# Performance work log

Measured on AMD Instinct MI355X. Metric: run time of the kernel, lower is better.

The kernel has to match this reference:

```python
import jax, jax.numpy as jnp
import numpy as np

H = 8      # num_attention_heads
DH = 96    # attention_head_size
LN_EPS = 1e-5


def setup_inputs() -> dict:
    key = jax.random.key(0)
    ks = jax.random.split(key, 12)
    B, S, D = 2, 768, 768
    sc = 0.02
    return {
        "hidden_states": jax.random.normal(ks[0], (B, S, D), jnp.float32),
        "distance_matrix": jax.random.uniform(ks[1], (B, S, S), jnp.float32) * 20.0,
        "angle_matrix": jax.random.uniform(ks[2], (B, S, S), jnp.float32) * np.pi,
        "attention_mask": jnp.ones((B, S), jnp.float32),
        "Wq": jax.random.normal(ks[3], (D, D), jnp.float32) * sc,
        "bq": jnp.zeros((D,), jnp.float32),
        "Wk": jax.random.normal(ks[4], (D, D), jnp.float32) * sc,
        "bk": jnp.zeros((D,), jnp.float32),
        "Wv": jax.random.normal(ks[5], (D, D), jnp.float32) * sc,
        "bv": jnp.zeros((D,), jnp.float32),
        "Wd": jax.random.normal(ks[6], (DH,), jnp.float32) * sc,
        "bd": jnp.zeros((DH,), jnp.float32),
        "Wa": jax.random.normal(ks[7], (DH,), jnp.float32) * sc,
        "ba": jnp.zeros((DH,), jnp.float32),
        "Wo": jax.random.normal(ks[8], (D, D), jnp.float32) * sc,
        "bo": jnp.zeros((D,), jnp.float32),
        "ln_g": jnp.ones((D,), jnp.float32),
        "ln_b": jnp.zeros((D,), jnp.float32),
    }


def _heads(x, B, S):
    # [B,S,D] -> [B,H,S,DH]
    return x.reshape(B, S, H, DH).transpose(0, 2, 1, 3)


def reference(hidden_states, distance_matrix, angle_matrix, attention_mask,
              Wq, bq, Wk, bk, Wv, bv, Wd, bd, Wa, ba, Wo, bo, ln_g, ln_b):
    B, S, D = hidden_states.shape
    q = _heads(hidden_states @ Wq.T + bq, B, S)   # [B,H,S,DH]
    k = _heads(hidden_states @ Wk.T + bk, B, S)
    v = _heads(hidden_states @ Wv.T + bv, B, S)

    scores = jnp.einsum('bhid,bhjd->bhij', q, k) / jnp.sqrt(jnp.float32(DH))

    # distance / angle relative-position biases: emb[b,i,j,:] = dist[b,i,j]*Wd + bd
    dist_emb = distance_matrix[..., None] * Wd + bd   # [B,S,S,DH]
    scores = scores + jnp.einsum('bhid,bijd->bhij', q, dist_emb)
    ang_emb = angle_matrix[..., None] * Wa + ba       # [B,S,S,DH]
    scores = scores + jnp.einsum('bhid,bijd->bhij', q, ang_emb)

    # key mask, broadcast over heads and query positions
    scores = scores + (1.0 - attention_mask)[:, None, None, :] * -10000.0

    probs = jax.nn.softmax(scores, axis=-1)           # [B,H,S,S]
    ctx = jnp.einsum('bhij,bhjd->bhid', probs, v)
    ctx = ctx.transpose(0, 2, 1, 3).reshape(B, S, D)  # [B,S,D]

    out = ctx @ Wo.T + bo
    x = out + hidden_states
    mu = jnp.mean(x, axis=-1, keepdims=True)
    var = jnp.var(x, axis=-1, keepdims=True)
    out = (x - mu) * jax.lax.rsqrt(var + LN_EPS) * ln_g + ln_b
    return out, probs
```

## Files before the change

kernel.cpp:

```cpp
#include <hip/hip_runtime.h>
#include <stdint.h>

#define B_  2
#define S_  768
#define D_  768
#define H_  8
#define DH_ 96

typedef unsigned short ushort_t;
typedef __bf16 bf16x8 __attribute__((ext_vector_type(8)));
typedef float  f32x4  __attribute__((ext_vector_type(4)));

__device__ inline ushort_t f2bf(float f) {
    union { float f; unsigned int u; } v; v.f = f;
    unsigned int u = v.u;
    unsigned int r = u + 0x7fffu + ((u >> 16) & 1u);
    return (ushort_t)(r >> 16);
}
__device__ inline float bf2f(ushort_t u) {
    union { unsigned int i; float f; } c; c.i = ((unsigned int)u) << 16;
    return c.f;
}

__device__ inline void glds16(const void* gp, void* lp) {
    auto g = reinterpret_cast<const __attribute__((address_space(1))) uint32_t*>(
        reinterpret_cast<uintptr_t>(gp));
    auto l = reinterpret_cast<__attribute__((address_space(3))) uint32_t*>(
        reinterpret_cast<uintptr_t>(lp));
    __builtin_amdgcn_global_load_lds(g, l, 16, 0, 0);
}

__global__ __launch_bounds__(256) void k_convert(
        const float* __restrict__ X, const float* __restrict__ Wq,
        const float* __restrict__ Wk, const float* __restrict__ Wv,
        const float* __restrict__ Wo,
        ushort_t* __restrict__ Xb, ushort_t* __restrict__ Wb) {
    const int NX4 = (B_ * S_ * D_) / 4;
    const int NW4 = (D_ * D_) / 4;
    int i = blockIdx.x * blockDim.x + threadIdx.x;
    float4 v;
    ushort_t* dst;
    if (i < NX4) {
        v = ((const float4*)X)[i];
        dst = Xb + i * 4;
    } else {
        int wi = i - NX4;
        int sel = wi / NW4;
        int off = wi - sel * NW4;
        const float* src = (sel == 0) ? Wq : (sel == 1) ? Wk : (sel == 2) ? Wv : Wo;
        v = ((const float4*)src)[off];
        dst = Wb + wi * 4;
    }
    ushort4 o;
    o.x = f2bf(v.x); o.y = f2bf(v.y); o.z = f2bf(v.z); o.w = f2bf(v.w);
    *(ushort4*)dst = o;
}

__device__ inline void gemm64_glds(
        const ushort_t* __restrict__ A, int lda,
        const ushort_t* __restrict__ Bt, int ldb,
        int K, int m0, int n0,
        ushort_t* As, ushort_t* Bs, f32x4 acc[2][2]) {
    const int tid  = threadIdx.x;
    const int lane = tid & 63, wave = tid >> 6;
    const int wm = (wave >> 1) * 32, wn = (wave & 1) * 32;
    const int fr = lane & 15, fk = (lane >> 4) * 8;
    const int sr = wave * 16 + (lane >> 2);
    const int sc = (lane & 3) * 8;
    const ushort_t* Ap = A  + (size_t)(m0 + sr) * lda + sc;
    const ushort_t* Bp = Bt + (size_t)(n0 + sr) * ldb + sc;
    ushort_t* AsW = As + wave * 512;
    ushort_t* BsW = Bs + wave * 512;
    for (int kt = 0; kt < K; kt += 32) {
        if (kt) __syncthreads();
        glds16(Ap + kt, AsW);
        glds16(Bp + kt, BsW);
        __syncthreads();
        bf16x8 a0 = *(const bf16x8*)&As[(wm      + fr) * 32 + fk];
        bf16x8 a1 = *(const bf16x8*)&As[(wm + 16 + fr) * 32 + fk];
        bf16x8 b0 = *(const bf16x8*)&Bs[(wn      + fr) * 32 + fk];
        bf16x8 b1 = *(const bf16x8*)&Bs[(wn + 16 + fr) * 32 + fk];
        acc[0][0] = __builtin_amdgcn_mfma_f32_16x16x32_bf16(a0, b0, acc[0][0], 0, 0, 0);
        acc[0][1] = __builtin_amdgcn_mfma_f32_16x16x32_bf16(a0, b1, acc[0][1], 0, 0, 0);
        acc[1][0] = __builtin_amdgcn_mfma_f32_16x16x32_bf16(a1, b0, acc[1][0], 0, 0, 0);
        acc[1][1] = __builtin_amdgcn_mfma_f32_16x16x32_bf16(a1, b1, acc[1][1], 0, 0, 0);
    }
}

__global__ __launch_bounds__(256) void k_qkv(
        const ushort_t* __restrict__ Xb, const ushort_t* __restrict__ Wb,
        const float* __restrict__ bq, const float* __restrict__ bk,
        const float* __restrict__ bv,
        ushort_t* __restrict__ Qb, ushort_t* __restrict__ Kb,
        ushort_t* __restrict__ Vtb) {
    __shared__ __align__(16) ushort_t As[128 * 32];
    __shared__ __align__(16) ushort_t Bs[64 * 32];
    f32x4 acc[4][2];
    #pragma unroll
    for (int i = 0; i < 4; i++)
        #pragma unroll
        for (int j = 0; j < 2; j++) acc[i][j] = (f32x4){0.f, 0.f, 0.f, 0.f};
    const int tid = threadIdx.x, lane = tid & 63, wave = tid >> 6;
    const int m0 = blockIdx.y * 128, n0 = blockIdx.x * 64;
    const int fr = lane & 15, fk = (lane >> 4) * 8;
    const int wm = (wave >> 1) * 64, wn = (wave & 1) * 32;
    const int sr = lane >> 2, sc = (lane & 3) * 8;
    const ushort_t* Ap0 = Xb + (size_t)(m0 + wave * 32 + sr) * D_ + sc;
    const ushort_t* Ap1 = Ap0 + 16 * D_;
    const ushort_t* Bp  = Wb + (size_t)(n0 + wave * 16 + sr) * D_ + sc;
    ushort_t* AsW0 = As + wave * 1024;
    ushort_t* AsW1 = As + wave * 1024 + 512;
    ushort_t* BsW  = Bs + wave * 512;
    for (int kt = 0; kt < D_; kt += 32) {
        if (kt) __syncthreads();
        glds16(Ap0 + kt, AsW0);
        glds16(Ap1 + kt, AsW1);
        glds16(Bp  + kt, BsW);
        __syncthreads();
        bf16x8 a[4], b[2];
        #pragma unroll
        for (int mi = 0; mi < 4; mi++)
            a[mi] = *(const bf16x8*)&As[(wm + mi * 16 + fr) * 32 + fk];
        #pragma unroll
        for (int ni = 0; ni < 2; ni++)
            b[ni] = *(const bf16x8*)&Bs[(wn + ni * 16 + fr) * 32 + fk];
        #pragma unroll
        for (int mi = 0; mi < 4; mi++)
            #pragma unroll
            for (int ni = 0; ni < 2; ni++)
                acc[mi][ni] = __builtin_amdgcn_mfma_f32_16x16x32_bf16(a[mi], b[ni], acc[mi][ni], 0, 0, 0);
    }
    #pragma unroll
    for (int ni = 0; ni < 2; ni++) {
        int gcol = n0 + wn + ni * 16 + fr;
        int g = gcol / D_, d768 = gcol - g * D_;
        int h = d768 / DH_, d = d768 - h * DH_;
        float bias = (g == 0 ? bq : (g == 1 ? bk : bv))[d768];
        #pragma unroll
        for (int mi = 0; mi < 4; mi++) {
            #pragma unroll
            for (int r = 0; r < 4; r++) {
                int grow = m0 + wm + mi * 16 + (lane >> 4) * 4 + r;
                int bidx = grow / S_, s = grow - bidx * S_;
                ushort_t ob = f2bf(acc[mi][ni][r] + bias);
                int bh = bidx * H_ + h;
                if (g == 0)      Qb[((size_t)bh * S_ + s) * DH_ + d] = ob;
                else if (g == 1) Kb[((size_t)bh * S_ + s) * DH_ + d] = ob;
                else             Vtb[((size_t)bh * DH_ + d) * S_ + s] = ob;
            }
        }
    }
}

__global__ __launch_bounds__(256) void k_qcoef(
        const ushort_t* __restrict__ Qb,
        const float* __restrict__ Wd, const float* __restrict__ bd,
        const float* __restrict__ Wa, const float* __restrict__ ba,
        float* __restrict__ qcoef) {
    const int wave = threadIdx.x >> 6, lane = threadIdx.x & 63;
    const int row = blockIdx.x * 4 + wave;
    const ushort_t* q = Qb + (size_t)row * DH_;
    float e0 = bf2f(q[lane]);
    float c0 = e0 * Wd[lane];
    float c1 = e0 * Wa[lane];
    float c2 = e0 * (bd[lane] + ba[lane]);
    if (lane < 32) {
        int d = 64 + lane;
        float e1 = bf2f(q[d]);
        c0 += e1 * Wd[d];
        c1 += e1 * Wa[d];
        c2 += e1 * (bd[d] + ba[d]);
    }
    #pragma unroll
    for (int o = 32; o > 0; o >>= 1) {
        c0 += __shfl_down(c0, o);
        c1 += __shfl_down(c1, o);
        c2 += __shfl_down(c2, o);
    }
    if (lane == 0) {
        qcoef[row * 3 + 0] = c0;
        qcoef[row * 3 + 1] = c1;
        qcoef[row * 3 + 2] = c2;
    }
}

__global__ __launch_bounds__(256) void k_scores(
        const ushort_t* __restrict__ Qb, const ushort_t* __restrict__ Kb,
        const float* __restrict__ qcoef,
        const float* __restrict__ distm, const float* __restrict__ angm,
        const float* __restrict__ mask, float* __restrict__ Sc) {
    __shared__ __align__(16) ushort_t As[64 * 32];
    __shared__ __align__(16) ushort_t Bs[64 * 32];
    f32x4 acc[2][2];
    #pragma unroll
    for (int i = 0; i < 2; i++)
        #pragma unroll
        for (int j = 0; j < 2; j++) acc[i][j] = (f32x4){0.f, 0.f, 0.f, 0.f};
    const int bh = blockIdx.z, b = bh >> 3;
    const ushort_t* A  = Qb + (size_t)bh * S_ * DH_;
    const ushort_t* Bt = Kb + (size_t)bh * S_ * DH_;
    const int m0 = blockIdx.y * 64, n0 = blockIdx.x * 64;
    gemm64_glds(A, DH_, Bt, DH_, DH_, m0, n0, As, Bs, acc);
    const int lane = threadIdx.x & 63, wave = threadIdx.x >> 6;
    const int wm = (wave >> 1) * 32, wn = (wave & 1) * 32;
    const float isq = 0.10206207261596577f;
    #pragma unroll
    for (int ni = 0; ni < 2; ni++) {
        int j = n0 + wn + ni * 16 + (lane & 15);
        float mb = (1.0f - mask[b * S_ + j]) * -10000.0f;
        #pragma unroll
        for (int mi = 0; mi < 2; mi++) {
            #pragma unroll
            for (int r = 0; r < 4; r++) {
                int i = m0 + wm + mi * 16 + (lane >> 4) * 4 + r;
                const float* qc = qcoef + ((size_t)bh * S_ + i) * 3;
                float dist = distm[((size_t)b * S_ + i) * S_ + j];
                float ang  = angm [((size_t)b * S_ + i) * S_ + j];
                Sc[((size_t)bh * S_ + i) * S_ + j] =
                    acc[mi][ni][r] * isq + dist * qc[0] + ang * qc[1] + qc[2] + mb;
            }
        }
    }
}

__global__ __launch_bounds__(256) void k_attnctx(
        const float* __restrict__ Sc, const ushort_t* __restrict__ Vtb,
        float* __restrict__ probs, ushort_t* __restrict__ Ctxb) {
    const int bh = blockIdx.y, b = bh >> 3, h = bh & 7;
    const int r0 = blockIdx.x * 32;
    const float* S = Sc + ((size_t)bh * S_ + r0) * S_;
    const ushort_t* Vt = Vtb + (size_t)bh * DH_ * S_;
    __shared__ float mrow[32], lrow[32];
    __shared__ __align__(16) ushort_t Ps[32 * 32];
    __shared__ __align__(16) ushort_t Vs[96 * 32];
    const int tid = threadIdx.x, lane = tid & 63, wave = tid >> 6;
    for (int rr = 0; rr < 8; rr++) {
        int row = wave * 8 + rr;
        const float* sr = S + (size_t)row * S_;
        float4 x0 = ((const float4*)sr)[lane];
        float4 x1 = ((const float4*)sr)[lane + 64];
        float4 x2 = ((const float4*)sr)[lane + 128];
        float mx = fmaxf(fmaxf(fmaxf(x0.x, x0.y), fmaxf(x0.z, x0.w)),
                   fmaxf(fmaxf(fmaxf(x1.x, x1.y), fmaxf(x1.z, x1.w)),
                         fmaxf(fmaxf(x2.x, x2.y), fmaxf(x2.z, x2.w))));
        #pragma unroll
        for (int o = 32; o > 0; o >>= 1) mx = fmaxf(mx, __shfl_down(mx, o));
        mx = __shfl(mx, 0);
        float s = __expf(x0.x - mx) + __expf(x0.y - mx) + __expf(x0.z - mx) + __expf(x0.w - mx)
                + __expf(x1.x - mx) + __expf(x1.y - mx) + __expf(x1.z - mx) + __expf(x1.w - mx)
                + __expf(x2.x - mx) + __expf(x2.y - mx) + __expf(x2.z - mx) + __expf(x2.w - mx);
        #pragma unroll
        for (int o = 32; o > 0; o >>= 1) s += __shfl_down(s, o);
        if (lane == 0) { mrow[row] = mx; lrow[row] = s; }
    }
    __syncthreads();
    const int mrow0 = (wave & 1) * 16;
    const int nb    = (wave >> 1) * 48;
    const int fr = lane & 15, fk = (lane >> 4) * 8;
    const int prow = tid >> 3, pc = (tid & 7) * 4;
    const float pm = mrow[prow];
    const float pinvl = 1.0f / lrow[prow];
    f32x4 acc[3];
    #pragma unroll
    for (int i = 0; i < 3; i++) acc[i] = (f32x4){0.f, 0.f, 0.f, 0.f};
    const int vr0 = tid >> 2, vc0 = (tid & 3) * 8;
    const int i1 = tid + 256;
    const int vr1 = i1 >> 2, vc1 = (i1 & 3) * 8;
    for (int kt = 0; kt < S_; kt += 32) {
        if (kt) __syncthreads();
        {
            float4 s4 = *(const float4*)(S + (size_t)prow * S_ + kt + pc);
            float e0 = __expf(s4.x - pm), e1 = __expf(s4.y - pm);
            float e2 = __expf(s4.z - pm), e3 = __expf(s4.w - pm);
            ushort4 pb;
            pb.x = f2bf(e0); pb.y = f2bf(e1); pb.z = f2bf(e2); pb.w = f2bf(e3);
            *(ushort4*)&Ps[prow * 32 + pc] = pb;
            float4 pn = {e0 * pinvl, e1 * pinvl, e2 * pinvl, e3 * pinvl};
            *(float4*)&probs[((size_t)bh * S_ + r0 + prow) * S_ + kt + pc] = pn;
        }
        *(uint4*)&Vs[vr0 * 32 + vc0] = *(const uint4*)(Vt + (size_t)vr0 * S_ + kt + vc0);
        if (i1 < 384)
            *(uint4*)&Vs[vr1 * 32 + vc1] = *(const uint4*)(Vt + (size_t)vr1 * S_ + kt + vc1);
        __syncthreads();
        bf16x8 a = *(const bf16x8*)&Ps[(mrow0 + fr) * 32 + fk];
        #pragma unroll
        for (int ni = 0; ni < 3; ni++) {
            bf16x8 bfr = *(const bf16x8*)&Vs[(nb + ni * 16 + fr) * 32 + fk];
            acc[ni] = __builtin_amdgcn_mfma_f32_16x16x32_bf16(a, bfr, acc[ni], 0, 0, 0);
        }
    }
    #pragma unroll
    for (int ni = 0; ni < 3; ni++) {
        int col = nb + ni * 16 + fr;
        #pragma unroll
        for (int r = 0; r < 4; r++) {
            int row = mrow0 + (lane >> 4) * 4 + r;
            float o = acc[ni][r] / lrow[row];
            Ctxb[((size_t)(b * S_ + r0 + row)) * D_ + h * DH_ + col] = f2bf(o);
        }
    }
}

__global__ __launch_bounds__(256) void k_out(
        const ushort_t* __restrict__ Ctxb, const ushort_t* __restrict__ Wob,
        const float* __restrict__ bo, const float* __restrict__ hidden,
        float* __restrict__ xbuf) {
    __shared__ __align__(16) ushort_t As[64 * 32];
    __shared__ __align__(16) ushort_t Bs[64 * 32];
    f32x4 acc[2][2];
    #pragma unroll
    for (int i = 0; i < 2; i++)
        #pragma unroll
        for (int j = 0; j < 2; j++) acc[i][j] = (f32x4){0.f, 0.f, 0.f, 0.f};
    const int m0 = blockIdx.y * 64, n0 = blockIdx.x * 64;
    gemm64_glds(Ctxb, D_, Wob, D_, D_, m0, n0, As, Bs, acc);
    const int lane = threadIdx.x & 63, wave = threadIdx.x >> 6;
    const int wm = (wave >> 1) * 32, wn = (wave & 1) * 32;
    #pragma unroll
    for (int ni = 0; ni < 2; ni++) {
        int gcol = n0 + wn + ni * 16 + (lane & 15);
        float bias = bo[gcol];
        #pragma unroll
        for (int mi = 0; mi < 2; mi++) {
            #pragma unroll
            for (int r = 0; r < 4; r++) {
                int grow = m0 + wm + mi * 16 + (lane >> 4) * 4 + r;
                xbuf[(size_t)grow * D_ + gcol] =
                    acc[mi][ni][r] + bias + hidden[(size_t)grow * D_ + gcol];
            }
        }
    }
}

__global__ __launch_bounds__(256) void k_ln(
        const float* __restrict__ xbuf, const float* __restrict__ g,
        const float* __restrict__ bb, float* __restrict__ out) {
    const float* x = xbuf + (size_t)blockIdx.x * D_;
    const int t = threadIdx.x;
    float a0 = x[t], a1 = x[t + 256], a2 = x[t + 512];
    float s = a0 + a1 + a2;
    float ss = a0 * a0 + a1 * a1 + a2 * a2;
    __shared__ float r1[4], r2[4];
    #pragma unroll
    for (int o = 32; o > 0; o >>= 1) { s += __shfl_down(s, o); ss += __shfl_down(ss, o); }
    if ((t & 63) == 0) { r1[t >> 6] = s; r2[t >> 6] = ss; }
    __syncthreads();
    float ts = r1[0] + r1[1] + r1[2] + r1[3];
    float tss = r2[0] + r2[1] + r2[2] + r2[3];
    float mu = ts * (1.0f / D_);
    float var = tss * (1.0f / D_) - mu * mu;
    float rstd = rsqrtf(var + 1e-5f);
    float* o = out + (size_t)blockIdx.x * D_;
    o[t]       = (a0 - mu) * rstd * g[t]       + bb[t];
    o[t + 256] = (a1 - mu) * rstd * g[t + 256] + bb[t + 256];
    o[t + 512] = (a2 - mu) * rstd * g[t + 512] + bb[t + 512];
}

extern "C" void kernel_launch(void* const* d_in, const int* in_sizes, int n_in,
                              void* d_out, int out_size, void* d_ws, size_t ws_size,
                              hipStream_t stream) {
    const float* X     = (const float*)d_in[0];
    const float* distm = (const float*)d_in[1];
    const float* angm  = (const float*)d_in[2];
    const float* mask  = (const float*)d_in[3];
    const float* Wq    = (const float*)d_in[4];
    const float* bq    = (const float*)d_in[5];
    const float* Wk    = (const float*)d_in[6];
    const float* bk    = (const float*)d_in[7];
    const float* Wv    = (const float*)d_in[8];
    const float* bv    = (const float*)d_in[9];
    const float* Wd    = (const float*)d_in[10];
    const float* bd    = (const float*)d_in[11];
    const float* Wa    = (const float*)d_in[12];
    const float* ba    = (const float*)d_in[13];
    const float* Wo    = (const float*)d_in[14];
    const float* bo    = (const float*)d_in[15];
    const float* ln_g  = (const float*)d_in[16];
    const float* ln_b  = (const float*)d_in[17];

    float* outp  = (float*)d_out;
    float* probs = (float*)d_out + (size_t)B_ * S_ * D_;

    char* ws = (char*)d_ws;
    ushort_t* Xb    = (ushort_t*)(ws + 0);
    ushort_t* Wb    = (ushort_t*)(ws + 2359296);
    ushort_t* Qb    = (ushort_t*)(ws + 7077888);
    ushort_t* Kb    = (ushort_t*)(ws + 9437184);
    ushort_t* Vtb   = (ushort_t*)(ws + 11796480);
    ushort_t* Ctxb  = (ushort_t*)(ws + 14155776);
    float*    qcoef = (float*)   (ws + 16515072);
    float*    xbuf  = (float*)   (ws + 16662528);
    float*    Sc    = (float*)   (ws + 21381120);

    k_convert<<<3456, 256, 0, stream>>>(X, Wq, Wk, Wv, Wo, Xb, Wb);
    k_qkv<<<dim3(36, 12), 256, 0, stream>>>(Xb, Wb, bq, bk, bv, Qb, Kb, Vtb);
    k_qcoef<<<3072, 256, 0, stream>>>(Qb, Wd, bd, Wa, ba, qcoef);
    k_scores<<<dim3(12, 12, 16), 256, 0, stream>>>(Qb, Kb, qcoef, distm, angm, mask, Sc);
    k_attnctx<<<dim3(24, 16), 256, 0, stream>>>(Sc, Vtb, probs, Ctxb);
    k_out<<<dim3(12, 24), 256, 0, stream>>>(Ctxb, Wb + (size_t)2304 * 768, bo, X, xbuf);
    k_ln<<<1536, 256, 0, stream>>>(xbuf, ln_g, ln_b, outp);
}
```

Measured before the change: 206.7 us.

## Fuse score computation, softmax and PV into one register-resident attention kernel

Result: faster. 180.8 us (-12.5%).

```diff
diff --git a/kernel.cpp b/kernel.cpp
--- a/kernel.cpp
+++ b/kernel.cpp
@@ -93,57 +93,31 @@
         const float* __restrict__ bv,
         ushort_t* __restrict__ Qb, ushort_t* __restrict__ Kb,
         ushort_t* __restrict__ Vtb) {
-    __shared__ __align__(16) ushort_t As[128 * 32];
+    __shared__ __align__(16) ushort_t As[64 * 32];
     __shared__ __align__(16) ushort_t Bs[64 * 32];
-    f32x4 acc[4][2];
-    #pragma unroll
-    for (int i = 0; i < 4; i++)
+    f32x4 acc[2][2];
+    #pragma unroll
+    for (int i = 0; i < 2; i++)
         #pragma unroll
         for (int j = 0; j < 2; j++) acc[i][j] = (f32x4){0.f, 0.f, 0.f, 0.f};
-    const int tid = threadIdx.x, lane = tid & 63, wave = tid >> 6;
-    const int m0 = blockIdx.y * 128, n0 = blockIdx.x * 64;
-    const int fr = lane & 15, fk = (lane >> 4) * 8;
-    const int wm = (wave >> 1) * 64, wn = (wave & 1) * 32;
-    const int sr = lane >> 2, sc = (lane & 3) * 8;
-    const ushort_t* Ap0 = Xb + (size_t)(m0 + wave * 32 + sr) * D_ + sc;
-    const ushort_t* Ap1 = Ap0 + 16 * D_;
-    const ushort_t* Bp  = Wb + (size_t)(n0 + wave * 16 + sr) * D_ + sc;
-    ushort_t* AsW0 = As + wave * 1024;
-    ushort_t* AsW1 = As + wave * 1024 + 512;
-    ushort_t* BsW  = Bs + wave * 512;
-    for (int kt = 0; kt < D_; kt += 32) {
-        if (kt) __syncthreads();
-        glds16(Ap0 + kt, AsW0);
-        glds16(Ap1 + kt, AsW1);
-        glds16(Bp  + kt, BsW);
-        __syncthreads();
-        bf16x8 a[4], b[2];
-        #pragma unroll
-        for (int mi = 0; mi < 4; mi++)
-            a[mi] = *(const bf16x8*)&As[(wm + mi * 16 + fr) * 32 + fk];
-        #pragma unroll
-        for (int ni = 0; ni < 2; ni++)
-            b[ni] = *(const bf16x8*)&Bs[(wn + ni * 16 + fr) * 32 + fk];
-        #pragma unroll
-        for (int mi = 0; mi < 4; mi++)
-            #pragma unroll
-            for (int ni = 0; ni < 2; ni++)
-                acc[mi][ni] = __builtin_amdgcn_mfma_f32_16x16x32_bf16(a[mi], b[ni], acc[mi][ni], 0, 0, 0);
-    }
+    const int m0 = blockIdx.y * 64, n0 = blockIdx.x * 64;
+    gemm64_glds(Xb, D_, Wb, D_, D_, m0, n0, As, Bs, acc);
+    const int lane = threadIdx.x & 63, wave = threadIdx.x >> 6;
+    const int wm = (wave >> 1) * 32, wn = (wave & 1) * 32;
     #pragma unroll
     for (int ni = 0; ni < 2; ni++) {
-        int gcol = n0 + wn + ni * 16 + fr;
+        int gcol = n0 + wn + ni * 16 + (lane & 15);
         int g = gcol / D_, d768 = gcol - g * D_;
         int h = d768 / DH_, d = d768 - h * DH_;
         float bias = (g == 0 ? bq : (g == 1 ? bk : bv))[d768];
         #pragma unroll
-        for (int mi = 0; mi < 4; mi++) {
+        for (int mi = 0; mi < 2; mi++) {
             #pragma unroll
             for (int r = 0; r < 4; r++) {
                 int grow = m0 + wm + mi * 16 + (lane >> 4) * 4 + r;
-                int bidx = grow / S_, s = grow - bidx * S_;
+                int b = grow / S_, s = grow - b * S_;
                 ushort_t ob = f2bf(acc[mi][ni][r] + bias);
-                int bh = bidx * H_ + h;
+                int bh = b * H_ + h;
                 if (g == 0)      Qb[((size_t)bh * S_ + s) * DH_ + d] = ob;
                 else if (g == 1) Kb[((size_t)bh * S_ + s) * DH_ + d] = ob;
                 else             Vtb[((size_t)bh * DH_ + d) * S_ + s] = ob;
@@ -184,119 +158,174 @@
     }
 }
 
-__global__ __launch_bounds__(256) void k_scores(
+#define L1B 29696
+__global__ __launch_bounds__(256) void k_flash(
         const ushort_t* __restrict__ Qb, const ushort_t* __restrict__ Kb,
-        const float* __restrict__ qcoef,
+        const ushort_t* __restrict__ Vtb, const float* __restrict__ qcoef,
         const float* __restrict__ distm, const float* __restrict__ angm,
-        const float* __restrict__ mask, float* __restrict__ Sc) {
-    __shared__ __align__(16) ushort_t As[64 * 32];
-    __shared__ __align__(16) ushort_t Bs[64 * 32];
-    f32x4 acc[2][2];
-    #pragma unroll
-    for (int i = 0; i < 2; i++)
-        #pragma unroll
-        for (int j = 0; j < 2; j++) acc[i][j] = (f32x4){0.f, 0.f, 0.f, 0.f};
-    const int bh = blockIdx.z, b = bh >> 3;
-    const ushort_t* A  = Qb + (size_t)bh * S_ * DH_;
-    const ushort_t* Bt = Kb + (size_t)bh * S_ * DH_;
-    const int m0 = blockIdx.y * 64, n0 = blockIdx.x * 64;
-    gemm64_glds(A, DH_, Bt, DH_, DH_, m0, n0, As, Bs, acc);
-    const int lane = threadIdx.x & 63, wave = threadIdx.x >> 6;
-    const int wm = (wave >> 1) * 32, wn = (wave & 1) * 32;
+        const float* __restrict__ mask,
+        float* __restrict__ probs, ushort_t* __restrict__ Ctxb) {
+    __shared__ __align__(16) char sm[2 * L1B + 640];
+    float* mstat = (float*)(sm + 2 * L1B);
+    float* lstat = (float*)(sm + 2 * L1B + 256);
+    float* linv  = (float*)(sm + 2 * L1B + 512);
+    const int idx = blockIdx.x;
+    const int h = idx / 48, rem = idx - h * 48;
+    const int b = rem / 24, r0 = (rem - b * 24) * 32;
+    const int bh = b * H_ + h;
+    const int tid = threadIdx.x, lane = tid & 63, w = tid >> 6;
+    const int frn = lane & 15, fko = (lane >> 4) * 8, frg4 = (lane >> 4) * 4;
+    const int rg = w & 1, cp = w >> 1;
+    const ushort_t* Qbh = Qb + (size_t)bh * S_ * DH_;
+    const ushort_t* Kbh = Kb + (size_t)bh * S_ * DH_;
+    const ushort_t* Vbh = Vtb + (size_t)bh * DH_ * S_;
+
+    bf16x8 aq[3];
+    {
+        const ushort_t* qp = Qbh + (size_t)(r0 + rg * 16 + frn) * DH_ + fko;
+        aq[0] = *(const bf16x8*)qp;
+        aq[1] = *(const bf16x8*)(qp + 32);
+        aq[2] = *(const bf16x8*)(qp + 64);
+    }
+    float qc0[4], qc1[4], qc2[4];
+    #pragma unroll
+    for (int r = 0; r < 4; r++) {
+        const float* qp = qcoef + ((size_t)bh * S_ + r0 + rg * 16 + frg4 + r) * 3;
+        qc0[r] = qp[0]; qc1[r] = qp[1]; qc2[r] = qp[2];
+    }
     const float isq = 0.10206207261596577f;
-    #pragma unroll
-    for (int ni = 0; ni < 2; ni++) {
-        int j = n0 + wn + ni * 16 + (lane & 15);
-        float mb = (1.0f - mask[b * S_ + j]) * -10000.0f;
-        #pragma unroll
-        for (int mi = 0; mi < 2; mi++) {
+
+    f32x4 acc[24];
+    #pragma unroll
+    for (int c = 0; c < 12; ++c) {
+        char* bufc = sm + (c & 1) * L1B;
+        ushort_t* Ks = (ushort_t*)bufc;
+        float* Dd = (float*)(bufc + 12288);
+        float* Da = (float*)(bufc + 20992);
+        #pragma unroll
+        for (int k = 0; k < 3; ++k) {
+            int i = tid + 256 * k;
+            int row = i / 12, cc = (i - row * 12) * 8;
+            *(uint4*)(Ks + row * 96 + cc) =
+                *(const uint4*)(Kbh + (size_t)(c * 64 + row) * DH_ + cc);
+        }
+        #pragma unroll
+        for (int k = 0; k < 2; ++k) {
+            int i = tid + 256 * k;
+            int row = i >> 4, c4 = (i & 15) * 4;
+            size_t src = ((size_t)b * S_ + r0 + row) * S_ + c * 64 + c4;
+            *(float4*)(Dd + row * 68 + c4) = *(const float4*)(distm + src);
+            *(float4*)(Da + row * 68 + c4) = *(const float4*)(angm + src);
+        }
+        __syncthreads();
+        #pragma unroll
+        for (int tt = 0; tt < 2; ++tt) {
+            const ushort_t* kp = Ks + (cp * 32 + tt * 16 + frn) * 96 + fko;
+            f32x4 ca = (f32x4){0.f, 0.f, 0.f, 0.f};
+            ca = __builtin_amdgcn_mfma_f32_16x16x32_bf16(aq[0], *(const bf16x8*)kp, ca, 0, 0, 0);
+            ca = __builtin_amdgcn_mfma_f32_16x16x32_bf16(aq[1], *(const bf16x8*)(kp + 32), ca, 0, 0, 0);
+            ca = __builtin_amdgcn_mfma_f32_16x16x32_bf16(aq[2], *(const bf16x8*)(kp + 64), ca, 0, 0, 0);
+            int jl = cp * 32 + tt * 16 + frn;
+            float mb = (1.0f - mask[b * S_ + c * 64 + jl]) * -10000.0f;
             #pragma unroll
-            for (int r = 0; r < 4; r++) {
-                int i = m0 + wm + mi * 16 + (lane >> 4) * 4 + r;
-                const float* qc = qcoef + ((size_t)bh * S_ + i) * 3;
-                float dist = distm[((size_t)b * S_ + i) * S_ + j];
-                float ang  = angm [((size_t)b * S_ + i) * S_ + j];
-                Sc[((size_t)bh * S_ + i) * S_ + j] =
-                    acc[mi][ni][r] * isq + dist * qc[0] + ang * qc[1] + qc[2] + mb;
+            for (int r = 0; r < 4; ++r) {
+                int rl = rg * 16 + frg4 + r;
+                acc[c * 2 + tt][r] = ca[r] * isq + Dd[rl * 68 + jl] * qc0[r]
+                                   + Da[rl * 68 + jl] * qc1[r] + qc2[r] + mb;
             }
         }
     }
-}
-
-__global__ __launch_bounds__(256) void k_attnctx(
-        const float* __restrict__ Sc, const ushort_t* __restrict__ Vtb,
-        float* __restrict__ probs, ushort_t* __restrict__ Ctxb) {
-    const int bh = blockIdx.y, b = bh >> 3, h = bh & 7;
-    const int r0 = blockIdx.x * 32;
-    const float* S = Sc + ((size_t)bh * S_ + r0) * S_;
-    const ushort_t* Vt = Vtb + (size_t)bh * DH_ * S_;
-    __shared__ float mrow[32], lrow[32];
-    __shared__ __align__(16) ushort_t Ps[32 * 32];
-    __shared__ __align__(16) ushort_t Vs[96 * 32];
-    const int tid = threadIdx.x, lane = tid & 63, wave = tid >> 6;
-    for (int rr = 0; rr < 8; rr++) {
-        int row = wave * 8 + rr;
-        const float* sr = S + (size_t)row * S_;
-        float4 x0 = ((const float4*)sr)[lane];
-        float4 x1 = ((const float4*)sr)[lane + 64];
-        float4 x2 = ((const float4*)sr)[lane + 128];
-        float mx = fmaxf(fmaxf(fmaxf(x0.x, x0.y), fmaxf(x0.z, x0.w)),
-                   fmaxf(fmaxf(fmaxf(x1.x, x1.y), fmaxf(x1.z, x1.w)),
-                         fmaxf(fmaxf(x2.x, x2.y), fmaxf(x2.z, x2.w))));
-        #pragma unroll
-        for (int o = 32; o > 0; o >>= 1) mx = fmaxf(mx, __shfl_down(mx, o));
-        mx = __shfl(mx, 0);
-        float s = __expf(x0.x - mx) + __expf(x0.y - mx) + __expf(x0.z - mx) + __expf(x0.w - mx)
-                + __expf(x1.x - mx) + __expf(x1.y - mx) + __expf(x1.z - mx) + __expf(x1.w - mx)
-                + __expf(x2.x - mx) + __expf(x2.y - mx) + __expf(x2.z - mx) + __expf(x2.w - mx);
-        #pragma unroll
-        for (int o = 32; o > 0; o >>= 1) s += __shfl_down(s, o);
-        if (lane == 0) { mrow[row] = mx; lrow[row] = s; }
-    }
+    float mx[4] = {-1e30f, -1e30f, -1e30f, -1e30f};
+    #pragma unroll
+    for (int t = 0; t < 24; t++)
+        #pragma unroll
+        for (int r = 0; r < 4; r++) mx[r] = fmaxf(mx[r], acc[t][r]);
+    #pragma unroll
+    for (int o = 1; o < 16; o <<= 1)
+        #pragma unroll
+        for (int r = 0; r < 4; r++) mx[r] = fmaxf(mx[r], __shfl_xor(mx[r], o));
+    if (frn == 0)
+        #pragma unroll
+        for (int r = 0; r < 4; r++) mstat[cp * 32 + rg * 16 + frg4 + r] = mx[r];
     __syncthreads();
-    const int mrow0 = (wave & 1) * 16;
-    const int nb    = (wave >> 1) * 48;
-    const int fr = lane & 15, fk = (lane >> 4) * 8;
-    const int prow = tid >> 3, pc = (tid & 7) * 4;
-    const float pm = mrow[prow];
-    const float pinvl = 1.0f / lrow[prow];
-    f32x4 acc[3];
-    #pragma unroll
-    for (int i = 0; i < 3; i++) acc[i] = (f32x4){0.f, 0.f, 0.f, 0.f};
-    const int vr0 = tid >> 2, vc0 = (tid & 3) * 8;
-    const int i1 = tid + 256;
-    const int vr1 = i1 >> 2, vc1 = (i1 & 3) * 8;
-    for (int kt = 0; kt < S_; kt += 32) {
-        if (kt) __syncthreads();
+    float mf[4], sum[4] = {0.f, 0.f, 0.f, 0.f};
+    #pragma unroll
+    for (int r = 0; r < 4; r++) {
+        int rl = rg * 16 + frg4 + r;
+        mf[r] = fmaxf(mstat[rl], mstat[32 + rl]);
+    }
+    #pragma unroll
+    for (int t = 0; t < 24; t++)
+        #pragma unroll
+        for (int r = 0; r < 4; r++) {
+            float e = __expf(acc[t][r] - mf[r]);
+            acc[t][r] = e;
+            sum[r] += e;
+        }
+    #pragma unroll
+    for (int o = 1; o < 16; o <<= 1)
+        #pragma unroll
+        for (int r = 0; r < 4; r++) sum[r] += __shfl_xor(sum[r], o);
+    if (frn == 0)
+        #pragma unroll
+        for (int r = 0; r < 4; r++) lstat[cp * 32 + rg * 16 + frg4 + r] = sum[r];
+    __syncthreads();
+    float inv[4];
+    #pragma unroll
+    for (int r = 0; r < 4; r++) {
+        int rl = rg * 16 + frg4 + r;
+        inv[r] = 1.0f / (lstat[rl] + lstat[32 + rl]);
+        if (cp == 0 && frn == 0) linv[rl] = inv[r];
+    }
+    __syncthreads();
+    f32x4 accO[3];
+    #pragma unroll
+    for (int i = 0; i < 3; i++) accO[i] = (f32x4){0.f, 0.f, 0.f, 0.f};
+    const int prow = tid >> 3, pc8 = (tid & 7) * 4;
+    float* pout = probs + ((size_t)bh * S_ + r0 + prow) * S_;
+    const int vrow = tid >> 2, vcv = (tid & 3) * 8;
+    const int vrow2 = (tid + 256) >> 2, vcv2 = ((tid + 256) & 3) * 8;
+    #pragma unroll
+    for (int s = 0; s < 24; ++s) {
+        ushort_t* Vs = (ushort_t*)(sm + (s & 1) * 7680);
+        ushort_t* Ps = (ushort_t*)(sm + 15360 + (s & 1) * 2560);
+        *(uint4*)(Vs + vrow * 40 + vcv) =
+            *(const uint4*)(Vbh + (size_t)vrow * S_ + s * 32 + vcv);
+        if (tid + 256 < 384)
+            *(uint4*)(Vs + vrow2 * 40 + vcv2) =
+                *(const uint4*)(Vbh + (size_t)vrow2 * S_ + s * 32 + vcv2);
+        if (cp == (s & 1)) {
+            #pragma unroll
+            for (int tt = 0; tt < 2; ++tt)
+                #pragma unroll
+                for (int r = 0; r < 4; ++r)
+                    Ps[(rg * 16 + frg4 + r) * 40 + tt * 16 + frn] =
+                        f2bf(acc[(s & ~1) + tt][r]);
+        }
+        __syncthreads();
         {
-            float4 s4 = *(const float4*)(S + (size_t)prow * S_ + kt + pc);
-            float e0 = __expf(s4.x - pm), e1 = __expf(s4.y - pm);
-            float e2 = __expf(s4.z - pm), e3 = __expf(s4.w - pm);
-            ushort4 pb;
-            pb.x = f2bf(e0); pb.y = f2bf(e1); pb.z = f2bf(e2); pb.w = f2bf(e3);
-            *(ushort4*)&Ps[prow * 32 + pc] = pb;
-            float4 pn = {e0 * pinvl, e1 * pinvl, e2 * pinvl, e3 * pinvl};
-            *(float4*)&probs[((size_t)bh * S_ + r0 + prow) * S_ + kt + pc] = pn;
-        }
-        *(uint4*)&Vs[vr0 * 32 + vc0] = *(const uint4*)(Vt + (size_t)vr0 * S_ + kt + vc0);
-        if (i1 < 384)
-            *(uint4*)&Vs[vr1 * 32 + vc1] = *(const uint4*)(Vt + (size_t)vr1 * S_ + kt + vc1);
-        __syncthreads();
-        bf16x8 a = *(const bf16x8*)&Ps[(mrow0 + fr) * 32 + fk];
-        #pragma unroll
-        for (int ni = 0; ni < 3; ni++) {
-            bf16x8 bfr = *(const bf16x8*)&Vs[(nb + ni * 16 + fr) * 32 + fk];
-            acc[ni] = __builtin_amdgcn_mfma_f32_16x16x32_bf16(a, bfr, acc[ni], 0, 0, 0);
-        }
-    }
-    #pragma unroll
-    for (int ni = 0; ni < 3; ni++) {
-        int col = nb + ni * 16 + fr;
-        #pragma unroll
-        for (int r = 0; r < 4; r++) {
-            int row = mrow0 + (lane >> 4) * 4 + r;
-            float o = acc[ni][r] / lrow[row];
-            Ctxb[((size_t)(b * S_ + r0 + row)) * D_ + h * DH_ + col] = f2bf(o);
+            float iv = linv[prow];
+            float4 p4;
+            p4.x = bf2f(Ps[prow * 40 + pc8 + 0]) * iv;
+            p4.y = bf2f(Ps[prow * 40 + pc8 + 1]) * iv;
+            p4.z = bf2f(Ps[prow * 40 + pc8 + 2]) * iv;
+            p4.w = bf2f(Ps[prow * 40 + pc8 + 3]) * iv;
+            *(float4*)(pout + s * 32 + pc8) = p4;
+        }
+        bf16x8 a = *(const bf16x8*)&Ps[(rg * 16 + frn) * 40 + fko];
+        #pragma unroll
+        for (int nt = 0; nt < 3; ++nt) {
+            bf16x8 v = *(const bf16x8*)&Vs[(cp * 48 + nt * 16 + frn) * 40 + fko];
+            accO[nt] = __builtin_amdgcn_mfma_f32_16x16x32_bf16(a, v, accO[nt], 0, 0, 0);
+        }
+    }
+    #pragma unroll
+    for (int nt = 0; nt < 3; ++nt) {
+        int col = h * DH_ + cp * 48 + nt * 16 + frn;
+        #pragma unroll
+        for (int r = 0; r < 4; ++r) {
+            int row = r0 + rg * 16 + frg4 + r;
+            Ctxb[((size_t)(b * S_ + row)) * D_ + col] = f2bf(accO[nt][r] * inv[r]);
         }
     }
 }
@@ -390,13 +419,11 @@
     ushort_t* Ctxb  = (ushort_t*)(ws + 14155776);
     float*    qcoef = (float*)   (ws + 16515072);
     float*    xbuf  = (float*)   (ws + 16662528);
-    float*    Sc    = (float*)   (ws + 21381120);
 
     k_convert<<<3456, 256, 0, stream>>>(X, Wq, Wk, Wv, Wo, Xb, Wb);
-    k_qkv<<<dim3(36, 12), 256, 0, stream>>>(Xb, Wb, bq, bk, bv, Qb, Kb, Vtb);
+    k_qkv<<<dim3(36, 24), 256, 0, stream>>>(Xb, Wb, bq, bk, bv, Qb, Kb, Vtb);
     k_qcoef<<<3072, 256, 0, stream>>>(Qb, Wd, bd, Wa, ba, qcoef);
-    k_scores<<<dim3(12, 12, 16), 256, 0, stream>>>(Qb, Kb, qcoef, distm, angm, mask, Sc);
-    k_attnctx<<<dim3(24, 16), 256, 0, stream>>>(Sc, Vtb, probs, Ctxb);
+    k_flash<<<384, 256, 0, stream>>>(Qb, Kb, Vtb, qcoef, distm, angm, mask, probs, Ctxb);
     k_out<<<dim3(12, 24), 256, 0, stream>>>(Ctxb, Wb + (size_t)2304 * 768, bo, X, xbuf);
     k_ln<<<1536, 256, 0, stream>>>(xbuf, ln_g, ln_b, outp);
 }
```
